# Performance work log

Measured on AMD Instinct MI355X. Metric: run time of the kernel, lower is better.

The kernel has to match this reference:

```python
import jax, jax.numpy as jnp
import numpy as np

NEG_SLOPE = 0.01  # torch nn.LeakyReLU default
N_NODES = 100000
N_EDGES = 500000
IN_DIM, OUT_DIM, EF_DIM, EMB_DIM = 128, 128, 64, 256


def leaky_relu(x):
    return jnp.where(x >= 0, x, NEG_SLOPE * x)


def setup_inputs() -> dict:
    key = jax.random.key(0)
    ks = jax.random.split(key, 8)
    s = 0.05
    nf = jax.random.normal(ks[0], (N_NODES, IN_DIM), dtype=jnp.float32)
    ef = jax.random.normal(ks[1], (N_EDGES, EF_DIM), dtype=jnp.float32)
    src = jax.random.randint(ks[2], (N_EDGES,), 0, N_NODES, dtype=jnp.int32)
    dst = jax.random.randint(ks[3], (N_EDGES,), 0, N_NODES, dtype=jnp.int32)
    # Linear weights stored as (in, out); y = x @ W. No biases (bias=False).
    We1 = jax.random.normal(ks[4], (2 * IN_DIM + EF_DIM, EMB_DIM), dtype=jnp.float32) * s
    We2 = jax.random.normal(ks[5], (EMB_DIM, OUT_DIM), dtype=jnp.float32) * s
    Wn1 = jax.random.normal(ks[6], (IN_DIM + OUT_DIM, EMB_DIM), dtype=jnp.float32) * s
    Wn2 = jax.random.normal(ks[7], (EMB_DIM, OUT_DIM), dtype=jnp.float32) * s
    return {"nf": nf, "ef": ef, "src": src, "dst": dst,
            "We1": We1, "We2": We2, "Wn1": Wn1, "Wn2": Wn2}


def reference(nf, ef, src, dst, We1, We2, Wn1, Wn2):
    # Symmetrize: add reversed edges carrying the same edge features.
    src_full = jnp.concatenate([src, dst])            # [2E]
    dst_full = jnp.concatenate([dst, src])            # [2E]
    ef_full = jnp.concatenate([ef, ef], axis=0)       # [2E, ef_dim]

    # message_func: MLP over [src_nf | dst_nf | ef]
    edge_in = jnp.concatenate([nf[src_full], nf[dst_full], ef_full], axis=-1)  # [2E, 2*in+ef]
    msg = leaky_relu(edge_in @ We1) @ We2              # [2E, out]

    # reduce_func: sum messages per destination node (zeros for isolated nodes)
    red = jax.ops.segment_sum(msg, dst_full, num_segments=nf.shape[0])  # [N, out]

    # apply_node_func: MLP over [nf | red_msg]
    node_in = jnp.concatenate([nf, red], axis=-1)      # [N, in+out]
    out_nf = leaky_relu(node_in @ Wn1) @ Wn2           # [N, out]
    return out_nf
```

## Files before the change

kernel.cpp:

```cpp
#include <hip/hip_runtime.h>
#include <hip/hip_bf16.h>
#include <string.h>


using f32x4  = __attribute__((ext_vector_type(4))) float;
using bf16x8 = __attribute__((ext_vector_type(8))) short;

#define LROW 72
#define CROW 132
#define P128 132
#define P256 264

__device__ __forceinline__ float lrelu(float x) { return x >= 0.f ? x : 0.01f * x; }

__device__ __forceinline__ ushort f2bf(float f) {
    union { float f; unsigned u; } v; v.f = f;
    unsigned u = v.u;
    return (ushort)((u + 0x7fffu + ((u >> 16) & 1u)) >> 16);
}
__device__ __forceinline__ float bf2f(ushort u) {
    union { unsigned u; float f; } v; v.u = ((unsigned)u) << 16; return v.f;
}

__device__ __forceinline__ void atomic_pk_add_bf16(void* addr, unsigned val) {
    asm volatile("global_atomic_pk_add_bf16 %0, %1, off" : : "v"(addr), "v"(val) : "memory");
}

__global__ __launch_bounds__(256) void gemm_ab(
    const ushort* __restrict__ X,
    const ushort* __restrict__ Wt,
    ushort* __restrict__ out)
{
    __shared__ ushort Xs[128 * P128];
    const int tid  = threadIdx.x;
    const int lane = tid & 63;
    const int wv   = tid >> 6;
    const int wm   = wv >> 1, wn = wv & 1;
    const int row0 = blockIdx.x * 128;

    #pragma unroll
    for (int q = 0; q < 8; ++q) {
        int idx = q * 256 + tid;
        int r = idx >> 4, c = idx & 15;
        *reinterpret_cast<uint4*>(&Xs[r * P128 + c * 8]) =
            *reinterpret_cast<const uint4*>(X + (size_t)(row0 + r) * 128 + c * 8);
    }
    __syncthreads();

    const int g8 = (lane >> 4) * 8;
    for (int cb = 0; cb < 4; ++cb) {
        f32x4 acc[4][4] = {};
        #pragma unroll
        for (int ks = 0; ks < 4; ++ks) {
            bf16x8 af[4], bf[4];
            #pragma unroll
            for (int i = 0; i < 4; ++i) {
                int mrow = wm * 64 + i * 16 + (lane & 15);
                af[i] = *reinterpret_cast<const bf16x8*>(&Xs[mrow * P128 + ks * 32 + g8]);
                int nc = cb * 128 + wn * 64 + i * 16 + (lane & 15);
                bf[i] = *reinterpret_cast<const bf16x8*>(Wt + (size_t)nc * 128 + ks * 32 + g8);
            }
            #pragma unroll
            for (int i = 0; i < 4; ++i)
                #pragma unroll
                for (int j = 0; j < 4; ++j)
                    acc[i][j] = __builtin_amdgcn_mfma_f32_16x16x32_bf16(af[i], bf[j], acc[i][j], 0, 0, 0);
        }
        #pragma unroll
        for (int i = 0; i < 4; ++i) {
            int gr0 = row0 + wm * 64 + i * 16 + ((lane >> 4) << 2);
            #pragma unroll
            for (int j = 0; j < 4; ++j) {
                int gc = cb * 128 + wn * 64 + j * 16 + (lane & 15);
                #pragma unroll
                for (int r = 0; r < 4; ++r)
                    out[(size_t)(gr0 + r) * 512 + gc] = f2bf(acc[i][j][r]);
            }
        }
    }
}

__global__ __launch_bounds__(256) void edge_fused(
    const ushort* __restrict__ efb,
    const ushort* __restrict__ Wet,
    const ushort* __restrict__ AB,
    const int* __restrict__ src, const int* __restrict__ dst,
    ushort* __restrict__ H,
    int E)
{
    __shared__ ushort lds[128 * LROW * 2];
    __shared__ int sd[256];

    const int tid  = threadIdx.x;
    const int lane = tid & 63;
    const int wv   = tid >> 6;
    const int wm   = wv >> 1, wn = wv & 1;
    const int bid  = blockIdx.x;
    const int eb   = (bid >> 1) * 128;
    const int col0 = (bid & 1) * 128;

    ushort* Xs = lds;
    ushort* Ws = lds + 128 * LROW;

    const int r_ = tid >> 3;
    const int kk = (tid & 7) * 8;
    uint4 xv[4], wvv[4];
    #pragma unroll
    for (int p = 0; p < 4; ++p) {
        int r = p * 32 + r_;
        xv[p]  = *reinterpret_cast<const uint4*>(efb + (size_t)(eb + r) * 64 + kk);
        wvv[p] = *reinterpret_cast<const uint4*>(Wet + (size_t)(col0 + r) * 64 + kk);
    }
    if (tid < 128) sd[tid] = (eb + tid < E)         ? src[eb + tid]         : -1;
    else           sd[tid] = (eb + (tid - 128) < E) ? dst[eb + (tid - 128)] : -1;
    #pragma unroll
    for (int p = 0; p < 4; ++p) {
        int r = p * 32 + r_;
        *reinterpret_cast<uint4*>(&Xs[r * LROW + kk]) = xv[p];
        *reinterpret_cast<uint4*>(&Ws[r * LROW + kk]) = wvv[p];
    }
    __syncthreads();

    f32x4 acc[4][4] = {};
    #pragma unroll
    for (int ks = 0; ks < 2; ++ks) {
        bf16x8 af[4], bfr[4];
        #pragma unroll
        for (int i = 0; i < 4; ++i) {
            int mrow = wm * 64 + i * 16 + (lane & 15);
            af[i]  = *reinterpret_cast<const bf16x8*>(&Xs[mrow * LROW + ks * 32 + (lane >> 4) * 8]);
            int ncol = wn * 64 + i * 16 + (lane & 15);
            bfr[i] = *reinterpret_cast<const bf16x8*>(&Ws[ncol * LROW + ks * 32 + (lane >> 4) * 8]);
        }
        #pragma unroll
        for (int i = 0; i < 4; ++i)
            #pragma unroll
            for (int j = 0; j < 4; ++j)
                acc[i][j] = __builtin_amdgcn_mfma_f32_16x16x32_bf16(af[i], bfr[j], acc[i][j], 0, 0, 0);
    }
    __syncthreads();

    ushort* Cs = lds;
    #pragma unroll
    for (int i = 0; i < 4; ++i) {
        int er0 = wm * 64 + i * 16 + ((lane >> 4) << 2);
        #pragma unroll
        for (int j = 0; j < 4; ++j) {
            int fc = wn * 64 + j * 16 + (lane & 15);
            #pragma unroll
            for (int r = 0; r < 4; ++r)
                Cs[(er0 + r) * CROW + fc] = f2bf(acc[i][j][r]);
        }
    }
    __syncthreads();

    const int jj = lane * 2;
    const ushort* ABj = AB + col0 + jj;
    ushort* Hj = H + col0 + jj;
    for (int p = 0; p < 32; ++p) {
        int ee = p * 4 + wv;
        int s = sd[ee], d = sd[128 + ee];
        if (s < 0) continue;
        ushort2 cv = *(const ushort2*)(&Cs[ee * CROW + jj]);
        ushort2 as = *(const ushort2*)(ABj + (size_t)s * 512);
        ushort2 bs = *(const ushort2*)(ABj + (size_t)s * 512 + 256);
        ushort2 ad = *(const ushort2*)(ABj + (size_t)d * 512);
        ushort2 bd = *(const ushort2*)(ABj + (size_t)d * 512 + 256);
        float c0 = bf2f(cv.x), c1 = bf2f(cv.y);
        ushort2 mf, mb;
        mf.x = f2bf(lrelu(bf2f(as.x) + bf2f(bd.x) + c0));
        mf.y = f2bf(lrelu(bf2f(as.y) + bf2f(bd.y) + c1));
        mb.x = f2bf(lrelu(bf2f(ad.x) + bf2f(bs.x) + c0));
        mb.y = f2bf(lrelu(bf2f(ad.y) + bf2f(bs.y) + c1));
        unsigned uf, ub;
        memcpy(&uf, &mf, 4); memcpy(&ub, &mb, 4);
        atomic_pk_add_bf16(Hj + (size_t)d * 256, uf);
        atomic_pk_add_bf16(Hj + (size_t)s * 256, ub);
    }
}

__global__ __launch_bounds__(256) void mlp_fused(
    const ushort* __restrict__ H,
    const ushort* __restrict__ nfb,
    const ushort* __restrict__ We2t,
    const ushort* __restrict__ Wn1t,
    const ushort* __restrict__ Wn2t,
    float* __restrict__ out, int Nreal)
{
    __shared__ ushort lds[128 * P256];
    ushort* Hs  = lds;
    ushort* Rs  = lds;
    ushort* Ns  = lds + 128 * P128;
    ushort* Hid = lds;

    const int tid  = threadIdx.x;
    const int lane = tid & 63;
    const int wv   = tid >> 6;
    const int wm   = wv >> 1, wn = wv & 1;
    const int row0 = blockIdx.x * 128;
    const int g8   = (lane >> 4) * 8;

    uint4 npre[8];
    #pragma unroll
    for (int q = 0; q < 8; ++q) {
        int idx = q * 256 + tid;
        int r = idx >> 4, c = idx & 15;
        npre[q] = *reinterpret_cast<const uint4*>(nfb + (size_t)(row0 + r) * 128 + c * 8);
    }
    #pragma unroll
    for (int q = 0; q < 16; ++q) {
        int idx = q * 256 + tid;
        int r = idx >> 5, c = idx & 31;
        *reinterpret_cast<uint4*>(&Hs[r * P256 + c * 8]) =
            *reinterpret_cast<const uint4*>(H + (size_t)(row0 + r) * 256 + c * 8);
    }
    __syncthreads();

    f32x4 acc[4][4] = {};
    #pragma unroll
    for (int ks = 0; ks < 8; ++ks) {
        bf16x8 af[4], bf[4];
        #pragma unroll
        for (int i = 0; i < 4; ++i) {
            int mrow = wm * 64 + i * 16 + (lane & 15);
            af[i] = *reinterpret_cast<const bf16x8*>(&Hs[mrow * P256 + ks * 32 + g8]);
            int nc = wn * 64 + i * 16 + (lane & 15);
            bf[i] = *reinterpret_cast<const bf16x8*>(We2t + (size_t)nc * 256 + ks * 32 + g8);
        }
        #pragma unroll
        for (int i = 0; i < 4; ++i)
            #pragma unroll
            for (int j = 0; j < 4; ++j)
                acc[i][j] = __builtin_amdgcn_mfma_f32_16x16x32_bf16(af[i], bf[j], acc[i][j], 0, 0, 0);
    }
    __syncthreads();

    #pragma unroll
    for (int i = 0; i < 4; ++i) {
        int er0 = wm * 64 + i * 16 + ((lane >> 4) << 2);
        #pragma unroll
        for (int j = 0; j < 4; ++j) {
            int fc = wn * 64 + j * 16 + (lane & 15);
            #pragma unroll
            for (int r = 0; r < 4; ++r)
                Rs[(er0 + r) * P128 + fc] = f2bf(acc[i][j][r]);
        }
    }
    #pragma unroll
    for (int q = 0; q < 8; ++q) {
        int idx = q * 256 + tid;
        int r = idx >> 4, c = idx & 15;
        *reinterpret_cast<uint4*>(&Ns[r * P128 + c * 8]) = npre[q];
    }
    __syncthreads();

    f32x4 a2[2][4][4] = {};
    #pragma unroll
    for (int cb = 0; cb < 2; ++cb) {
        #pragma unroll
        for (int ks = 0; ks < 8; ++ks) {
            bf16x8 af[4], bf[4];
            #pragma unroll
            for (int i = 0; i < 4; ++i) {
                int mrow = wm * 64 + i * 16 + (lane & 15);
                af[i] = (ks < 4)
                    ? *reinterpret_cast<const bf16x8*>(&Ns[mrow * P128 + ks * 32 + g8])
                    : *reinterpret_cast<const bf16x8*>(&Rs[mrow * P128 + (ks - 4) * 32 + g8]);
                int nc = cb * 128 + wn * 64 + i * 16 + (lane & 15);
                bf[i] = *reinterpret_cast<const bf16x8*>(Wn1t + (size_t)nc * 256 + ks * 32 + g8);
            }
            #pragma unroll
            for (int i = 0; i < 4; ++i)
                #pragma unroll
                for (int j = 0; j < 4; ++j)
                    a2[cb][i][j] = __builtin_amdgcn_mfma_f32_16x16x32_bf16(af[i], bf[j], a2[cb][i][j], 0, 0, 0);
        }
    }
    __syncthreads();

    #pragma unroll
    for (int cb = 0; cb < 2; ++cb)
        #pragma unroll
        for (int i = 0; i < 4; ++i) {
            int er0 = wm * 64 + i * 16 + ((lane >> 4) << 2);
            #pragma unroll
            for (int j = 0; j < 4; ++j) {
                int fc = cb * 128 + wn * 64 + j * 16 + (lane & 15);
                #pragma unroll
                for (int r = 0; r < 4; ++r)
                    Hid[(er0 + r) * P256 + fc] = f2bf(lrelu(a2[cb][i][j][r]));
            }
        }
    __syncthreads();

    f32x4 a3[4][4] = {};
    #pragma unroll
    for (int ks = 0; ks < 8; ++ks) {
        bf16x8 af[4], bf[4];
        #pragma unroll
        for (int i = 0; i < 4; ++i) {
            int mrow = wm * 64 + i * 16 + (lane & 15);
            af[i] = *reinterpret_cast<const bf16x8*>(&Hid[mrow * P256 + ks * 32 + g8]);
            int nc = wn * 64 + i * 16 + (lane & 15);
            bf[i] = *reinterpret_cast<const bf16x8*>(Wn2t + (size_t)nc * 256 + ks * 32 + g8);
        }
        #pragma unroll
        for (int i = 0; i < 4; ++i)
            #pragma unroll
            for (int j = 0; j < 4; ++j)
                a3[i][j] = __builtin_amdgcn_mfma_f32_16x16x32_bf16(af[i], bf[j], a3[i][j], 0, 0, 0);
    }
    #pragma unroll
    for (int i = 0; i < 4; ++i) {
        int gr0 = row0 + wm * 64 + i * 16 + ((lane >> 4) << 2);
        #pragma unroll
        for (int j = 0; j < 4; ++j) {
            int gc = wn * 64 + j * 16 + (lane & 15);
            #pragma unroll
            for (int r = 0; r < 4; ++r) {
                int gr = gr0 + r;
                if (gr < Nreal) out[(size_t)gr * 128 + gc] = a3[i][j][r];
            }
        }
    }
}

__global__ __launch_bounds__(256) void cvt_pad(
    const float* __restrict__ x, ushort* __restrict__ y, size_t n_real, size_t n_pad)
{
    size_t i = ((size_t)blockIdx.x * 256 + threadIdx.x) * 4;
    if (i >= n_pad) return;
    ushort4 o;
    if (i < n_real) {
        float4 v = *(const float4*)(x + i);
        o.x = f2bf(v.x); o.y = f2bf(v.y); o.z = f2bf(v.z); o.w = f2bf(v.w);
    } else { o.x = 0; o.y = 0; o.z = 0; o.w = 0; }
    *(ushort4*)(y + i) = o;
}

__global__ __launch_bounds__(256) void wcvt(
    const float* __restrict__ We1, const float* __restrict__ We2,
    const float* __restrict__ Wn1, const float* __restrict__ Wn2,
    ushort* __restrict__ Wabt, ushort* __restrict__ Wet, ushort* __restrict__ We2t,
    ushort* __restrict__ Wn1t, ushort* __restrict__ Wn2t)
{
    int idx = blockIdx.x * 256 + threadIdx.x;
    switch (blockIdx.y) {
    case 0: if (idx < 256*128) { int n = idx >> 7, k = idx & 127; Wabt[idx]            = f2bf(We1[k * 256 + n]); } break;
    case 1: if (idx < 256*128) { int n = idx >> 7, k = idx & 127; Wabt[32768 + idx]    = f2bf(We1[(128 + k) * 256 + n]); } break;
    case 2: if (idx < 256*64)  { int n = idx >> 6, k = idx & 63;  Wet[idx]             = f2bf(We1[(256 + k) * 256 + n]); } break;
    case 3: if (idx < 128*256) { int n = idx >> 8, k = idx & 255; We2t[idx]            = f2bf(We2[k * 128 + n]); } break;
    case 4: if (idx < 256*256) { int n = idx >> 8, k = idx & 255; Wn1t[idx]            = f2bf(Wn1[k * 256 + n]); } break;
    case 5: if (idx < 128*256) { int n = idx >> 8, k = idx & 255; Wn2t[idx]            = f2bf(Wn2[k * 128 + n]); } break;
    }
}

extern "C" void kernel_launch(void* const* d_in, const int* in_sizes, int n_in,
                              void* d_out, int out_size, void* d_ws, size_t ws_size,
                              hipStream_t stream) {
    const float* nf  = (const float*)d_in[0];
    const float* ef  = (const float*)d_in[1];
    const int*   src = (const int*)d_in[2];
    const int*   dst = (const int*)d_in[3];
    const float* We1 = (const float*)d_in[4];
    const float* We2 = (const float*)d_in[5];
    const float* Wn1 = (const float*)d_in[6];
    const float* Wn2 = (const float*)d_in[7];
    float* out = (float*)d_out;

    const int  N  = in_sizes[0] / 128;
    const int  E  = in_sizes[2];
    const int  Np = (N + 127) & ~127;
    const long Ep = ((long)E + 127) & ~127L;

    char* p = (char*)d_ws;
    auto alloc = [&](size_t bytes) { char* r = p; p += (bytes + 255) & ~(size_t)255; return r; };
    ushort* AB   = (ushort*)alloc((size_t)Np * 512 * 2);
    ushort* H    = (ushort*)alloc((size_t)Np * 256 * 2);
    ushort* nfb  = (ushort*)alloc((size_t)Np * 128 * 2);
    ushort* efb  = (ushort*)alloc((size_t)Ep * 64 * 2);
    ushort* Wabt = (ushort*)alloc(65536 * 2);
    ushort* Wet  = (ushort*)alloc(16384 * 2);
    ushort* We2t = (ushort*)alloc(32768 * 2);
    ushort* Wn1t = (ushort*)alloc(65536 * 2);
    ushort* Wn2t = (ushort*)alloc(32768 * 2);

    dim3 blk(256);

    wcvt<<<dim3(256, 6), blk, 0, stream>>>(We1, We2, Wn1, Wn2, Wabt, Wet, We2t, Wn1t, Wn2t);
    cvt_pad<<<dim3((unsigned)((size_t)Np * 128 / 1024)), blk, 0, stream>>>(nf, nfb, (size_t)N * 128, (size_t)Np * 128);
    cvt_pad<<<dim3((unsigned)((size_t)Ep * 64 / 1024)), blk, 0, stream>>>(ef, efb, (size_t)E * 64, (size_t)Ep * 64);

    gemm_ab<<<dim3(Np / 128), blk, 0, stream>>>(nfb, Wabt, AB);

    hipMemsetAsync(H, 0, (size_t)Np * 256 * 2, stream);

    edge_fused<<<dim3((unsigned)(Ep / 128 * 2)), blk, 0, stream>>>(
        efb, Wet, AB, src, dst, H, E);

    mlp_fused<<<dim3(Np / 128), blk, 0, stream>>>(H, nfb, We2t, Wn1t, Wn2t, out, N);
}
```

Before: 830.0 us.

## Apply second edge MLP layer per edge before scatter to halve atomics

```diff
diff --git a/kernel.cpp b/kernel.cpp
--- a/kernel.cpp
+++ b/kernel.cpp
@@ -7,7 +7,8 @@
 using bf16x8 = __attribute__((ext_vector_type(8))) short;
 
 #define LROW 72
-#define CROW 132
+#define CSROW 264
+#define YROW 132
 #define P128 132
 #define P256 264
 
@@ -80,117 +81,138 @@
     }
 }
 
-__global__ __launch_bounds__(256) void edge_fused(
+__global__ __launch_bounds__(256) void edge_proj(
     const ushort* __restrict__ efb,
     const ushort* __restrict__ Wet,
+    const ushort* __restrict__ We2t,
     const ushort* __restrict__ AB,
     const int* __restrict__ src, const int* __restrict__ dst,
     ushort* __restrict__ H,
     int E)
 {
-    __shared__ ushort lds[128 * LROW * 2];
-    __shared__ int sd[256];
+    __shared__ ushort Cs[128 * YROW];
+    __shared__ ushort efs[64 * LROW];
+    __shared__ int sd[128];
 
     const int tid  = threadIdx.x;
     const int lane = tid & 63;
     const int wv   = tid >> 6;
     const int wm   = wv >> 1, wn = wv & 1;
-    const int bid  = blockIdx.x;
-    const int eb   = (bid >> 1) * 128;
-    const int col0 = (bid & 1) * 128;
-
-    ushort* Xs = lds;
-    ushort* Ws = lds + 128 * LROW;
-
-    const int r_ = tid >> 3;
-    const int kk = (tid & 7) * 8;
-    uint4 xv[4], wvv[4];
-    #pragma unroll
-    for (int p = 0; p < 4; ++p) {
-        int r = p * 32 + r_;
-        xv[p]  = *reinterpret_cast<const uint4*>(efb + (size_t)(eb + r) * 64 + kk);
-        wvv[p] = *reinterpret_cast<const uint4*>(Wet + (size_t)(col0 + r) * 64 + kk);
-    }
-    if (tid < 128) sd[tid] = (eb + tid < E)         ? src[eb + tid]         : -1;
-    else           sd[tid] = (eb + (tid - 128) < E) ? dst[eb + (tid - 128)] : -1;
-    #pragma unroll
-    for (int p = 0; p < 4; ++p) {
-        int r = p * 32 + r_;
-        *reinterpret_cast<uint4*>(&Xs[r * LROW + kk]) = xv[p];
-        *reinterpret_cast<uint4*>(&Ws[r * LROW + kk]) = wvv[p];
+    const int eb   = blockIdx.x * 64;
+    const int g8   = (lane >> 4) * 8;
+
+    #pragma unroll
+    for (int q = 0; q < 2; ++q) {
+        int idx = q * 256 + tid;
+        int r = idx >> 3, c = (idx & 7) * 8;
+        *reinterpret_cast<uint4*>(&efs[r * LROW + c]) =
+            *reinterpret_cast<const uint4*>(efb + (size_t)(eb + r) * 64 + c);
+    }
+    if (tid < 64)       sd[tid] = (eb + tid < E) ? src[eb + tid] : -1;
+    else if (tid < 128) sd[tid] = (eb + tid - 64 < E) ? dst[eb + tid - 64] : -1;
+    __syncthreads();
+
+    f32x4 accc[4][4] = {};
+    #pragma unroll
+    for (int ks = 0; ks < 2; ++ks) {
+        bf16x8 af[4], bf[4];
+        #pragma unroll
+        for (int i = 0; i < 4; ++i) {
+            int er = i * 16 + (lane & 15);
+            af[i] = *reinterpret_cast<const bf16x8*>(&efs[er * LROW + ks * 32 + g8]);
+            int nc = wv * 64 + i * 16 + (lane & 15);
+            bf[i] = *reinterpret_cast<const bf16x8*>(Wet + (size_t)nc * 64 + ks * 32 + g8);
+        }
+        #pragma unroll
+        for (int i = 0; i < 4; ++i)
+            #pragma unroll
+            for (int j = 0; j < 4; ++j)
+                accc[i][j] = __builtin_amdgcn_mfma_f32_16x16x32_bf16(af[i], bf[j], accc[i][j], 0, 0, 0);
+    }
+    #pragma unroll
+    for (int i = 0; i < 4; ++i) {
+        int er0 = i * 16 + ((lane >> 4) << 2);
+        #pragma unroll
+        for (int j = 0; j < 4; ++j) {
+            int fc = wv * 64 + j * 16 + (lane & 15);
+            #pragma unroll
+            for (int r = 0; r < 4; ++r)
+                Cs[(er0 + r) * CSROW + fc] = f2bf(accc[i][j][r]);
+        }
     }
     __syncthreads();
 
     f32x4 acc[4][4] = {};
     #pragma unroll
-    for (int ks = 0; ks < 2; ++ks) {
-        bf16x8 af[4], bfr[4];
-        #pragma unroll
-        for (int i = 0; i < 4; ++i) {
-            int mrow = wm * 64 + i * 16 + (lane & 15);
-            af[i]  = *reinterpret_cast<const bf16x8*>(&Xs[mrow * LROW + ks * 32 + (lane >> 4) * 8]);
-            int ncol = wn * 64 + i * 16 + (lane & 15);
-            bfr[i] = *reinterpret_cast<const bf16x8*>(&Ws[ncol * LROW + ks * 32 + (lane >> 4) * 8]);
+    for (int ks = 0; ks < 8; ++ks) {
+        bf16x8 mf[4], wf[4];
+        #pragma unroll
+        for (int i = 0; i < 4; ++i) {
+            int el = i * 16 + (lane & 15);
+            int a_ = wm ? sd[64 + el] : sd[el];
+            int b_ = wm ? sd[el]      : sd[64 + el];
+            if (a_ < 0) a_ = 0;
+            if (b_ < 0) b_ = 0;
+            int k = ks * 32 + g8;
+            bf16x8 a8 = *reinterpret_cast<const bf16x8*>(AB + (size_t)a_ * 512 + k);
+            bf16x8 b8 = *reinterpret_cast<const bf16x8*>(AB + (size_t)b_ * 512 + 256 + k);
+            bf16x8 c8 = *reinterpret_cast<const bf16x8*>(&Cs[el * CSROW + k]);
+            bf16x8 m8;
+            #pragma unroll
+            for (int t = 0; t < 8; ++t) {
+                float f = lrelu(bf2f((ushort)a8[t]) + bf2f((ushort)b8[t]) + bf2f((ushort)c8[t]));
+                m8[t] = (short)f2bf(f);
+            }
+            mf[i] = m8;
+        }
+        #pragma unroll
+        for (int j = 0; j < 4; ++j) {
+            int nc = wn * 64 + j * 16 + (lane & 15);
+            wf[j] = *reinterpret_cast<const bf16x8*>(We2t + (size_t)nc * 256 + ks * 32 + g8);
         }
         #pragma unroll
         for (int i = 0; i < 4; ++i)
             #pragma unroll
             for (int j = 0; j < 4; ++j)
-                acc[i][j] = __builtin_amdgcn_mfma_f32_16x16x32_bf16(af[i], bfr[j], acc[i][j], 0, 0, 0);
-    }
-    __syncthreads();
-
-    ushort* Cs = lds;
+                acc[i][j] = __builtin_amdgcn_mfma_f32_16x16x32_bf16(mf[i], wf[j], acc[i][j], 0, 0, 0);
+    }
+    __syncthreads();
+
+    ushort* Ys = Cs;
     #pragma unroll
     for (int i = 0; i < 4; ++i) {
-        int er0 = wm * 64 + i * 16 + ((lane >> 4) << 2);
+        int yr0 = wm * 64 + i * 16 + ((lane >> 4) << 2);
         #pragma unroll
         for (int j = 0; j < 4; ++j) {
-            int fc = wn * 64 + j * 16 + (lane & 15);
+            int yc = wn * 64 + j * 16 + (lane & 15);
             #pragma unroll
             for (int r = 0; r < 4; ++r)
-                Cs[(er0 + r) * CROW + fc] = f2bf(acc[i][j][r]);
-        }
-    }
-    __syncthreads();
-
-    const int jj = lane * 2;
-    const ushort* ABj = AB + col0 + jj;
-    ushort* Hj = H + col0 + jj;
-    for (int p = 0; p < 32; ++p) {
-        int ee = p * 4 + wv;
-        int s = sd[ee], d = sd[128 + ee];
-        if (s < 0) continue;
-        ushort2 cv = *(const ushort2*)(&Cs[ee * CROW + jj]);
-        ushort2 as = *(const ushort2*)(ABj + (size_t)s * 512);
-        ushort2 bs = *(const ushort2*)(ABj + (size_t)s * 512 + 256);
-        ushort2 ad = *(const ushort2*)(ABj + (size_t)d * 512);
-        ushort2 bd = *(const ushort2*)(ABj + (size_t)d * 512 + 256);
-        float c0 = bf2f(cv.x), c1 = bf2f(cv.y);
-        ushort2 mf, mb;
-        mf.x = f2bf(lrelu(bf2f(as.x) + bf2f(bd.x) + c0));
-        mf.y = f2bf(lrelu(bf2f(as.y) + bf2f(bd.y) + c1));
-        mb.x = f2bf(lrelu(bf2f(ad.x) + bf2f(bs.x) + c0));
-        mb.y = f2bf(lrelu(bf2f(ad.y) + bf2f(bs.y) + c1));
-        unsigned uf, ub;
-        memcpy(&uf, &mf, 4); memcpy(&ub, &mb, 4);
-        atomic_pk_add_bf16(Hj + (size_t)d * 256, uf);
-        atomic_pk_add_bf16(Hj + (size_t)s * 256, ub);
+                Ys[(yr0 + r) * YROW + yc] = f2bf(acc[i][j][r]);
+        }
+    }
+    __syncthreads();
+
+    #pragma unroll
+    for (int q = 0; q < 32; ++q) {
+        int row = wv * 32 + q;
+        int node = (row < 64) ? sd[64 + row] : sd[row - 64];
+        if (node < 0) continue;
+        ushort2 yv = *(const ushort2*)(&Ys[row * YROW + lane * 2]);
+        unsigned uv; memcpy(&uv, &yv, 4);
+        atomic_pk_add_bf16(H + (size_t)node * 128 + lane * 2, uv);
     }
 }
 
 __global__ __launch_bounds__(256) void mlp_fused(
     const ushort* __restrict__ H,
     const ushort* __restrict__ nfb,
-    const ushort* __restrict__ We2t,
     const ushort* __restrict__ Wn1t,
     const ushort* __restrict__ Wn2t,
     float* __restrict__ out, int Nreal)
 {
     __shared__ ushort lds[128 * P256];
-    ushort* Hs  = lds;
-    ushort* Rs  = lds;
-    ushort* Ns  = lds + 128 * P128;
+    ushort* Ns  = lds;
+    ushort* Rs  = lds + 128 * P128;
     ushort* Hid = lds;
 
     const int tid  = threadIdx.x;
@@ -200,57 +222,14 @@
     const int row0 = blockIdx.x * 128;
     const int g8   = (lane >> 4) * 8;
 
-    uint4 npre[8];
     #pragma unroll
     for (int q = 0; q < 8; ++q) {
         int idx = q * 256 + tid;
-        int r = idx >> 4, c = idx & 15;
-        npre[q] = *reinterpret_cast<const uint4*>(nfb + (size_t)(row0 + r) * 128 + c * 8);
-    }
-    #pragma unroll
-    for (int q = 0; q < 16; ++q) {
-        int idx = q * 256 + tid;
-        int r = idx >> 5, c = idx & 31;
-        *reinterpret_cast<uint4*>(&Hs[r * P256 + c * 8]) =
-            *reinterpret_cast<const uint4*>(H + (size_t)(row0 + r) * 256 + c * 8);
-    }
-    __syncthreads();
-
-    f32x4 acc[4][4] = {};
-    #pragma unroll
-    for (int ks = 0; ks < 8; ++ks) {
-        bf16x8 af[4], bf[4];
-        #pragma unroll
-        for (int i = 0; i < 4; ++i) {
-            int mrow = wm * 64 + i * 16 + (lane & 15);
-            af[i] = *reinterpret_cast<const bf16x8*>(&Hs[mrow * P256 + ks * 32 + g8]);
-            int nc = wn * 64 + i * 16 + (lane & 15);
-            bf[i] = *reinterpret_cast<const bf16x8*>(We2t + (size_t)nc * 256 + ks * 32 + g8);
-        }
-        #pragma unroll
-        for (int i = 0; i < 4; ++i)
-            #pragma unroll
-            for (int j = 0; j < 4; ++j)
-                acc[i][j] = __builtin_amdgcn_mfma_f32_16x16x32_bf16(af[i], bf[j], acc[i][j], 0, 0, 0);
-    }
-    __syncthreads();
-
-    #pragma unroll
-    for (int i = 0; i < 4; ++i) {
-        int er0 = wm * 64 + i * 16 + ((lane >> 4) << 2);
-        #pragma unroll
-        for (int j = 0; j < 4; ++j) {
-            int fc = wn * 64 + j * 16 + (lane & 15);
-            #pragma unroll
-            for (int r = 0; r < 4; ++r)
-                Rs[(er0 + r) * P128 + fc] = f2bf(acc[i][j][r]);
-        }
-    }
-    #pragma unroll
-    for (int q = 0; q < 8; ++q) {
-        int idx = q * 256 + tid;
-        int r = idx >> 4, c = idx & 15;
-        *reinterpret_cast<uint4*>(&Ns[r * P128 + c * 8]) = npre[q];
+        int r = idx >> 4, c = (idx & 15) * 8;
+        *reinterpret_cast<uint4*>(&Ns[r * P128 + c]) =
+            *reinterpret_cast<const uint4*>(nfb + (size_t)(row0 + r) * 128 + c);
+        *reinterpret_cast<uint4*>(&Rs[r * P128 + c]) =
+            *reinterpret_cast<const uint4*>(H + (size_t)(row0 + r) * 128 + c);
     }
     __syncthreads();
 
@@ -376,7 +355,7 @@
     char* p = (char*)d_ws;
     auto alloc = [&](size_t bytes) { char* r = p; p += (bytes + 255) & ~(size_t)255; return r; };
     ushort* AB   = (ushort*)alloc((size_t)Np * 512 * 2);
-    ushort* H    = (ushort*)alloc((size_t)Np * 256 * 2);
+    ushort* H    = (ushort*)alloc((size_t)Np * 128 * 2);
     ushort* nfb  = (ushort*)alloc((size_t)Np * 128 * 2);
     ushort* efb  = (ushort*)alloc((size_t)Ep * 64 * 2);
     ushort* Wabt = (ushort*)alloc(65536 * 2);
@@ -393,10 +372,10 @@
 
     gemm_ab<<<dim3(Np / 128), blk, 0, stream>>>(nfb, Wabt, AB);
 
-    hipMemsetAsync(H, 0, (size_t)Np * 256 * 2, stream);
-
-    edge_fused<<<dim3((unsigned)(Ep / 128 * 2)), blk, 0, stream>>>(
-        efb, Wet, AB, src, dst, H, E);
-
-    mlp_fused<<<dim3(Np / 128), blk, 0, stream>>>(H, nfb, We2t, Wn1t, Wn2t, out, N);
-}
+    hipMemsetAsync(H, 0, (size_t)Np * 128 * 2, stream);
+
+    edge_proj<<<dim3((unsigned)(Ep / 64)), blk, 0, stream>>>(
+        efb, Wet, We2t, AB, src, dst, H, E);
+
+    mlp_fused<<<dim3(Np / 128), blk, 0, stream>>>(H, nfb, Wn1t, Wn2t, out, N);
+}
```

Result: slower. 914.0 us (+10.1%).
